# Performance work log

Hardware: AMD Instinct MI355X
Metric: run time of the kernel (lower is better)

## Reference

```python
import jax, jax.numpy as jnp
import numpy as np

ALPHA = 0.5  # init alpha
B, T, D, H = 32, 1024, 512, 512


def _cell(x, h, c, wih, whh, bih, bhh):
    # PyTorch LSTM cell: gates in i, f, g, o order
    g = x @ wih.T + bih + h @ whh.T + bhh  # (B, 4H)
    i, f, gg, o = jnp.split(g, 4, axis=-1)
    c2 = jax.nn.sigmoid(f) * c + jax.nn.sigmoid(i) * jnp.tanh(gg)
    h2 = jax.nn.sigmoid(o) * jnp.tanh(c2)
    return h2, c2


def setup_inputs() -> dict:
    key = jax.random.key(0)
    ks = jax.random.split(key, 9)
    s = 1.0 / np.sqrt(H)  # torch default init scale
    u = lambda k, shp: jax.random.uniform(k, shp, jnp.float32, -s, s)
    return {
        "u_sequence": jax.random.normal(ks[0], (B, T, D), jnp.float32),
        "w_ih_f": u(ks[1], (4 * H, D)),
        "w_hh_f": u(ks[2], (4 * H, H)),
        "b_ih_f": u(ks[3], (4 * H,)),
        "b_hh_f": u(ks[4], (4 * H,)),
        "w_ih_b": u(ks[5], (4 * H, D)),
        "w_hh_b": u(ks[6], (4 * H, H)),
        "b_ih_b": u(ks[7], (4 * H,)),
        "b_hh_b": u(ks[8], (4 * H,)),
    }


def reference(u_sequence, w_ih_f, w_hh_f, b_ih_f, b_hh_f,
              w_ih_b, w_hh_b, b_ih_b, b_hh_b):
    # Per timestep the original calls the bidirectional LSTM on a length-1
    # slice: both directions reduce to a single cell step on the same input.
    # Hidden/cell state (2, B, H) is carried across timesteps.
    pf = (w_ih_f, w_hh_f, b_ih_f, b_hh_f)
    pb = (w_ih_b, w_hh_b, b_ih_b, b_hh_b)
    Bn, Tn, Dn = u_sequence.shape
    Hn = w_hh_f.shape[1]
    z = jnp.zeros((Bn, Hn), u_sequence.dtype)

    def bi_step(x, hf, cf, hb, cb):
        hf2, cf2 = _cell(x, hf, cf, *pf)
        hb2, cb2 = _cell(x, hb, cb, *pb)
        # lstm_out[:, 0, :] == concat(h_fwd, h_bwd) for seq_len == 1
        return jnp.concatenate([hf2, hb2], axis=-1), hf2, cf2, hb2, cb2

    def step(carry, u_t):  # u_t: (B, D)
        hf, cf, hb, cb = carry
        out1, hf1, cf1, hb1, cb1 = bi_step(u_t, hf, cf, hb, cb)
        x_hat = out1[:, -1:]                 # last channel scalar, (B, 1)
        x_hat_prime = u_t + x_hat            # broadcast -> (B, D)
        out2, hf2, cf2, hb2, cb2 = bi_step(x_hat_prime, hf1, cf1, hb1, cb1)
        x_hat_next = out2[:, -1:]
        out = u_t + (1.0 - ALPHA) * x_hat_prime + ALPHA * x_hat_next
        return (hf2, cf2, hb2, cb2), out

    u_tm = jnp.swapaxes(u_sequence, 0, 1)    # (T, B, D)
    _, outs = jax.lax.scan(step, (z, z, z, z), u_tm)
    return jnp.swapaxes(outs, 0, 1)          # (B, T, D)
```

## Files before the change

### kernel.cpp

```cpp
#include <hip/hip_runtime.h>
#include <cstdint>
#include <cstddef>

#define BB 32
#define TT 1024
#define DD 512
#define HH 512
#define NBLK 64
#define NTHR 512

typedef __bf16 bf16x8 __attribute__((ext_vector_type(8)));
typedef float  f32x4  __attribute__((ext_vector_type(4)));
typedef unsigned long long u64;

#define HFRAG_OFF 0
#define XHAT_OFF  131072
#define IFLAG_OFF 393216
#define VFLAG_OFF 394240

#define AT_LOAD(p)     __hip_atomic_load((p),      __ATOMIC_RELAXED, __HIP_MEMORY_SCOPE_AGENT)
#define AT_STORE(p, v) __hip_atomic_store((p), (v), __ATOMIC_RELAXED, __HIP_MEMORY_SCOPE_AGENT)

__device__ __forceinline__ float sigm(float x) {
    return 1.f / (1.f + __expf(-x));
}
__device__ __forceinline__ float tanh_fast(float x) {
    x = fminf(15.f, fmaxf(-15.f, x));
    float e = __expf(2.f * x);
    return (e - 1.f) / (e + 1.f);
}


__device__ __forceinline__ void arrive_flag(int* iflags, int bid) {
    __builtin_amdgcn_s_waitcnt(0);
    __syncthreads();
    if (threadIdx.x == 0) AT_STORE(&iflags[bid], 1);
}
__device__ __forceinline__ void wait_flag(const int* iflags) {
    if (threadIdx.x < 64) {
        for (;;) {
            int v = AT_LOAD(&iflags[threadIdx.x]);
            if (__all(v >= 1)) break;
            __builtin_amdgcn_s_sleep(1);
        }
    }
    __syncthreads();
}

__device__ __forceinline__ void publish(int* vf, int bid, int n) {
    __builtin_amdgcn_s_waitcnt(0);
    __syncthreads();
    if (threadIdx.x == 0) AT_STORE(&vf[bid], n);
}
__device__ __forceinline__ void wait_ver(const int* vf, int n) {
    if (threadIdx.x < 64) {
        for (;;) {
            int v = AT_LOAD(&vf[threadIdx.x]);
            if (__all(v >= n)) break;
        }
    }
    __syncthreads();
}

#define UGEMM_HALF(tt, S0)                                                    \
  {                                                                           \
    const float* ub = u + (size_t)bc * (TT * DD) + (size_t)(tt) * DD + quad * 8; \
    _Pragma("unroll")                                                         \
    for (int i8 = 0; i8 < 8; ++i8) {                                          \
      const int s = (S0) + i8;                                                \
      const float4* p = (const float4*)(ub + s * 32);                         \
      float4 x0 = p[0], x1 = p[1];                                            \
      bf16x8 uf;                                                              \
      uf[0] = (__bf16)x0.x; uf[1] = (__bf16)x0.y;                             \
      uf[2] = (__bf16)x0.z; uf[3] = (__bf16)x0.w;                             \
      uf[4] = (__bf16)x1.x; uf[5] = (__bf16)x1.y;                             \
      uf[6] = (__bf16)x1.z; uf[7] = (__bf16)x1.w;                             \
      if (s & 1) un1 = __builtin_amdgcn_mfma_f32_16x16x32_bf16(wihF[s], uf, un1, 0, 0, 0); \
      else       un0 = __builtin_amdgcn_mfma_f32_16x16x32_bf16(wihF[s], uf, un0, 0, 0, 0); \
    }                                                                         \
  }

__global__ __launch_bounds__(NTHR, 1) void lstm_persistent(
    const float* __restrict__ u,
    const float* __restrict__ wih_f, const float* __restrict__ whh_f,
    const float* __restrict__ bih_f, const float* __restrict__ bhh_f,
    const float* __restrict__ wih_b, const float* __restrict__ whh_b,
    const float* __restrict__ bih_b, const float* __restrict__ bhh_b,
    unsigned short* __restrict__ hfrag, float* __restrict__ xhat,
    int* __restrict__ iflags, int* __restrict__ vflags)
{
    const int bid  = blockIdx.x;
    const int k0   = bid << 3;
    const int tid  = threadIdx.x;
    const int wid  = tid >> 6;
    const int dir  = wid >> 2;
    const int mi   = (wid >> 1) & 1;
    const int ni   = wid & 1;
    const int lane = tid & 63;
    const int quad = lane >> 4;
    const int l16  = lane & 15;

    const float* wih = dir ? wih_b : wih_f;
    const float* whh = dir ? whh_b : whh_f;
    const float* bih = dir ? bih_b : bih_f;
    const float* bhh = dir ? bhh_b : bhh_f;

    bf16x8 wihF[16], whhF[16];
    {
        const int jg = (l16 >> 2) * HH + (k0 + 4 * mi) + (l16 & 3);
        #pragma unroll
        for (int s = 0; s < 16; ++s) {
            const float* p = wih + (size_t)jg * DD + s * 32 + quad * 8;
            const float* q = whh + (size_t)jg * HH + s * 32 + quad * 8;
            bf16x8 a, b;
            #pragma unroll
            for (int i = 0; i < 8; ++i) { a[i] = (__bf16)p[i]; b[i] = (__bf16)q[i]; }
            wihF[s] = a;
            whhF[s] = b;
        }
    }

    const int kc = k0 + 4 * mi + quad;
    const int bc = ni * 16 + l16;

    float rsv[4], biasv[4];
    {
        float rs = 0.f;
        #pragma unroll
        for (int s = 0; s < 16; ++s)
            #pragma unroll
            for (int i = 0; i < 8; ++i) rs += (float)wihF[s][i];
        rs += __shfl_xor(rs, 16);
        rs += __shfl_xor(rs, 32);
        #pragma unroll
        for (int g = 0; g < 4; ++g) {
            rsv[g]   = __shfl(rs, g * 4 + quad);
            const int j = g * HH + kc;
            biasv[g] = bih[j] + bhh[j];
        }
    }

    const int sw = kc >> 5, qw = (kc >> 3) & 3, iw = kc & 7;
    const int lanew = qw * 16 + l16;
    unsigned* hfrag32 = (unsigned*)hfrag;
    const int ws32_0 = (((((dir * 2 + 0) * 2 + ni) * 16 + sw) * 64 + lanew) * 8 + iw) >> 1;
    const int ws32_1 = ws32_0 + (2 * 16 * 64 * 8 >> 1);
    const u64* h64 = (const u64*)hfrag;
    const int rbA = ((dir * 2 + 0) * 2 + ni) * 2048 + lane * 2;
    const int rbB = ((dir * 2 + 1) * 2 + ni) * 2048 + lane * 2;

    if (!(quad & 1)) AT_STORE(&hfrag32[ws32_0], 0u);
    if (bid == 0 && tid < 64) AT_STORE(&vflags[tid], 0);

    __shared__ __align__(16) float gbuf[8][16][20];

    arrive_flag(iflags, bid);
    f32x4 un0 = (f32x4){0.f, 0.f, 0.f, 0.f};
    f32x4 un1 = (f32x4){0.f, 0.f, 0.f, 0.f};
    UGEMM_HALF(0, 0);
    UGEMM_HALF(0, 8);
    wait_flag(iflags);

    f32x4 gih = un0 + un1;
    float c = 0.f;
    int n = 1;

    for (int t = 0; t < TT; ++t) {
        #pragma unroll 1
        for (int pass = 0; pass < 2; ++pass, ++n) {
            const int bufR = (t * 2 + pass) & 1;
            float xc = 0.f;
            if (pass) xc = AT_LOAD(&xhat[t * BB + bc]);

            u64 ha[16], hb[16];
            {
                const int rb = bufR ? rbB : rbA;
                #pragma unroll
                for (int s = 0; s < 16; ++s) {
                    ha[s] = AT_LOAD(&h64[rb + s * 128]);
                    hb[s] = AT_LOAD(&h64[rb + s * 128 + 1]);
                }
            }
            f32x4 acc0 = gih;
            f32x4 acc1 = (f32x4){0.f, 0.f, 0.f, 0.f};
            #pragma unroll
            for (int s = 0; s < 16; ++s) {
                union { u64 q[2]; bf16x8 v; } cvt;
                cvt.q[0] = ha[s]; cvt.q[1] = hb[s];
                if (s & 1) acc1 = __builtin_amdgcn_mfma_f32_16x16x32_bf16(whhF[s], cvt.v, acc1, 0, 0, 0);
                else       acc0 = __builtin_amdgcn_mfma_f32_16x16x32_bf16(whhF[s], cvt.v, acc0, 0, 0, 0);
            }
            f32x4 acc = acc0 + acc1;

            float4 gw; gw.x = acc[0]; gw.y = acc[1]; gw.z = acc[2]; gw.w = acc[3];
            *(float4*)&gbuf[wid][l16][quad * 4] = gw;
            __syncthreads();
            float gI = gbuf[wid][l16][ 0 + quad] + biasv[0] + xc * rsv[0];
            float gF = gbuf[wid][l16][ 4 + quad] + biasv[1] + xc * rsv[1];
            float gG = gbuf[wid][l16][ 8 + quad] + biasv[2] + xc * rsv[2];
            float gO = gbuf[wid][l16][12 + quad] + biasv[3] + xc * rsv[3];

            float ig = sigm(gI), fg = sigm(gF), gg = tanh_fast(gG), og = sigm(gO);
            c = fg * c + ig * gg;
            float h = og * tanh_fast(c);

            float hp = __shfl_xor(h, 16);
            if (dir == 1 && kc == (HH - 1))
                AT_STORE(&xhat[pass * (TT * BB) + t * BB + bc], h);
            if (!(quad & 1)) {
                unsigned lo = (unsigned)__builtin_bit_cast(unsigned short, (__bf16)h);
                unsigned hi = (unsigned)__builtin_bit_cast(unsigned short, (__bf16)hp);
                AT_STORE(&hfrag32[bufR ? ws32_0 : ws32_1], lo | (hi << 16));
            }

            publish(vflags, bid, n);
            if (t + 1 < TT) {
                if (pass == 0) {
                    un0 = (f32x4){0.f, 0.f, 0.f, 0.f};
                    un1 = (f32x4){0.f, 0.f, 0.f, 0.f};
                    UGEMM_HALF(t + 1, 0);
                } else {
                    UGEMM_HALF(t + 1, 8);
                }
            }
            wait_ver(vflags, n);
        }
        gih = un0 + un1;
    }
}

__global__ void epilogue(const float* __restrict__ u, const float* __restrict__ xhat,
                         float* __restrict__ out)
{
    const int i = blockIdx.x * blockDim.x + threadIdx.x;
    const float4 uv = ((const float4*)u)[i];
    const int bt = i >> 7;
    const int t = bt & (TT - 1);
    const int b = bt >> 10;
    const float s = 0.5f * (xhat[t * BB + b] + xhat[TT * BB + t * BB + b]);
    float4 o;
    o.x = 1.5f * uv.x + s;
    o.y = 1.5f * uv.y + s;
    o.z = 1.5f * uv.z + s;
    o.w = 1.5f * uv.w + s;
    ((float4*)out)[i] = o;
}

extern "C" void kernel_launch(void* const* d_in, const int* in_sizes, int n_in,
                              void* d_out, int out_size, void* d_ws, size_t ws_size,
                              hipStream_t stream) {
    const float* u     = (const float*)d_in[0];
    const float* wih_f = (const float*)d_in[1];
    const float* whh_f = (const float*)d_in[2];
    const float* bih_f = (const float*)d_in[3];
    const float* bhh_f = (const float*)d_in[4];
    const float* wih_b = (const float*)d_in[5];
    const float* whh_b = (const float*)d_in[6];
    const float* bih_b = (const float*)d_in[7];
    const float* bhh_b = (const float*)d_in[8];

    char* ws = (char*)d_ws;
    unsigned short* hfrag = (unsigned short*)(ws + HFRAG_OFF);
    float* xhat           = (float*)(ws + XHAT_OFF);
    int* iflags           = (int*)(ws + IFLAG_OFF);
    int* vflags           = (int*)(ws + VFLAG_OFF);

    lstm_persistent<<<NBLK, NTHR, 0, stream>>>(
        u, wih_f, whh_f, bih_f, bhh_f, wih_b, whh_b, bih_b, bhh_b,
        hfrag, xhat, iflags, vflags);

    const int n4 = BB * TT * DD / 4;
    epilogue<<<n4 / 256, 256, 0, stream>>>(u, xhat, (float*)d_out);
}
```

Before: 15.28 ms.

## Replace per-step grid barrier with NaN-sentinel data-flag polling on 4-slot ring

Removes the publish/wait_ver version-flag grid barrier each pass. Instead, hidden-state fragments and the x_hat scalar live in a 4-deep ring buffer whose slots are pre-cleared to a NaN sentinel. Readers poll the data itself until no sentinel remains, and writers clear the slot two steps ahead. This drops a barrier round trip and block-wide syncs from the recurrent critical path. In exchange it relies on the sentinel never colliding with real bf16 data and on relaxed-atomic ordering, and it polls without sleep.

```diff
diff --git a/kernel.cpp b/kernel.cpp
--- a/kernel.cpp
+++ b/kernel.cpp
@@ -13,10 +13,13 @@
 typedef float  f32x4  __attribute__((ext_vector_type(4)));
 typedef unsigned long long u64;
 
+#define CLR32  0x7FC07FC0u
+#define CLRF   0x7FC00000u
+
 #define HFRAG_OFF 0
-#define XHAT_OFF  131072
-#define IFLAG_OFF 393216
-#define VFLAG_OFF 394240
+#define XHAT_OFF  262144
+#define XRING_OFF 524288
+#define IFLAG_OFF 524800
 
 #define AT_LOAD(p)     __hip_atomic_load((p),      __ATOMIC_RELAXED, __HIP_MEMORY_SCOPE_AGENT)
 #define AT_STORE(p, v) __hip_atomic_store((p), (v), __ATOMIC_RELAXED, __HIP_MEMORY_SCOPE_AGENT)
@@ -29,7 +32,6 @@
     float e = __expf(2.f * x);
     return (e - 1.f) / (e + 1.f);
 }
-
 
 __device__ __forceinline__ void arrive_flag(int* iflags, int bid) {
     __builtin_amdgcn_s_waitcnt(0);
@@ -42,21 +44,6 @@
             int v = AT_LOAD(&iflags[threadIdx.x]);
             if (__all(v >= 1)) break;
             __builtin_amdgcn_s_sleep(1);
-        }
-    }
-    __syncthreads();
-}
-
-__device__ __forceinline__ void publish(int* vf, int bid, int n) {
-    __builtin_amdgcn_s_waitcnt(0);
-    __syncthreads();
-    if (threadIdx.x == 0) AT_STORE(&vf[bid], n);
-}
-__device__ __forceinline__ void wait_ver(const int* vf, int n) {
-    if (threadIdx.x < 64) {
-        for (;;) {
-            int v = AT_LOAD(&vf[threadIdx.x]);
-            if (__all(v >= n)) break;
         }
     }
     __syncthreads();
@@ -87,7 +74,7 @@
     const float* __restrict__ wih_b, const float* __restrict__ whh_b,
     const float* __restrict__ bih_b, const float* __restrict__ bhh_b,
     unsigned short* __restrict__ hfrag, float* __restrict__ xhat,
-    int* __restrict__ iflags, int* __restrict__ vflags)
+    unsigned* __restrict__ xring, int* __restrict__ iflags)
 {
     const int bid  = blockIdx.x;
     const int k0   = bid << 3;
@@ -143,14 +130,19 @@
     const int sw = kc >> 5, qw = (kc >> 3) & 3, iw = kc & 7;
     const int lanew = qw * 16 + l16;
     unsigned* hfrag32 = (unsigned*)hfrag;
-    const int ws32_0 = (((((dir * 2 + 0) * 2 + ni) * 16 + sw) * 64 + lanew) * 8 + iw) >> 1;
-    const int ws32_1 = ws32_0 + (2 * 16 * 64 * 8 >> 1);
+    const int ws32_rel = (((((dir) * 2 + ni) * 16 + sw) * 64 + lanew) * 8 + iw) >> 1;
     const u64* h64 = (const u64*)hfrag;
-    const int rbA = ((dir * 2 + 0) * 2 + ni) * 2048 + lane * 2;
-    const int rbB = ((dir * 2 + 1) * 2 + ni) * 2048 + lane * 2;
-
-    if (!(quad & 1)) AT_STORE(&hfrag32[ws32_0], 0u);
-    if (bid == 0 && tid < 64) AT_STORE(&vflags[tid], 0);
+
+    if (!(quad & 1)) {
+        AT_STORE(&hfrag32[0 * 16384 + ws32_rel], 0u);
+        AT_STORE(&hfrag32[1 * 16384 + ws32_rel], CLR32);
+        AT_STORE(&hfrag32[2 * 16384 + ws32_rel], CLR32);
+        AT_STORE(&hfrag32[3 * 16384 + ws32_rel], CLR32);
+    }
+    if (dir == 1 && kc == (HH - 1)) {
+        #pragma unroll
+        for (int b2 = 0; b2 < 4; ++b2) AT_STORE(&xring[b2 * BB + bc], CLRF);
+    }
 
     __shared__ __align__(16) float gbuf[8][16][20];
 
@@ -163,24 +155,39 @@
 
     f32x4 gih = un0 + un1;
     float c = 0.f;
-    int n = 1;
 
     for (int t = 0; t < TT; ++t) {
         #pragma unroll 1
-        for (int pass = 0; pass < 2; ++pass, ++n) {
-            const int bufR = (t * 2 + pass) & 1;
-            float xc = 0.f;
-            if (pass) xc = AT_LOAD(&xhat[t * BB + bc]);
+        for (int pass = 0; pass < 2; ++pass) {
+            const int n    = t * 2 + pass;
+            const int rbuf = n & 3;
+            const int wbuf = (n + 1) & 3;
+            const int cbuf = (n + 3) & 3;
 
             u64 ha[16], hb[16];
-            {
-                const int rb = bufR ? rbB : rbA;
+            unsigned rdys = 0;
+            bool xok = (pass == 0);
+            unsigned xbits = 0;
+            const int rb = ((rbuf * 2 + dir) * 2 + ni) * 2048 + lane * 2;
+            for (;;) {
                 #pragma unroll
-                for (int s = 0; s < 16; ++s) {
+                for (int s = 0; s < 16; ++s) if (!((rdys >> s) & 1)) {
                     ha[s] = AT_LOAD(&h64[rb + s * 128]);
                     hb[s] = AT_LOAD(&h64[rb + s * 128 + 1]);
                 }
-            }
+                if (!xok) xbits = AT_LOAD(&xring[rbuf * BB + bc]);
+                bool allr = true;
+                #pragma unroll
+                for (int s = 0; s < 16; ++s) if (!((rdys >> s) & 1)) {
+                    bool ok = ((unsigned)ha[s] != CLR32) && ((unsigned)(ha[s] >> 32) != CLR32)
+                           && ((unsigned)hb[s] != CLR32) && ((unsigned)(hb[s] >> 32) != CLR32);
+                    if (__all(ok)) rdys |= (1u << s); else allr = false;
+                }
+                if (!xok) { if (__all(xbits != CLRF)) xok = true; else allr = false; }
+                if (allr && xok) break;
+            }
+            const float xc = pass ? __builtin_bit_cast(float, xbits) : 0.f;
+
             f32x4 acc0 = gih;
             f32x4 acc1 = (f32x4){0.f, 0.f, 0.f, 0.f};
             #pragma unroll
@@ -205,15 +212,20 @@
             float h = og * tanh_fast(c);
 
             float hp = __shfl_xor(h, 16);
-            if (dir == 1 && kc == (HH - 1))
-                AT_STORE(&xhat[pass * (TT * BB) + t * BB + bc], h);
+            if (dir == 1 && kc == (HH - 1)) {
+                xhat[pass * (TT * BB) + t * BB + bc] = h;
+                AT_STORE(&xring[wbuf * BB + bc], __builtin_bit_cast(unsigned, h));
+            }
             if (!(quad & 1)) {
                 unsigned lo = (unsigned)__builtin_bit_cast(unsigned short, (__bf16)h);
                 unsigned hi = (unsigned)__builtin_bit_cast(unsigned short, (__bf16)hp);
-                AT_STORE(&hfrag32[bufR ? ws32_0 : ws32_1], lo | (hi << 16));
-            }
-
-            publish(vflags, bid, n);
+                AT_STORE(&hfrag32[wbuf * 16384 + ws32_rel], lo | (hi << 16));
+            }
+
+            if (!(quad & 1)) AT_STORE(&hfrag32[cbuf * 16384 + ws32_rel], CLR32);
+            if (dir == 1 && kc == (HH - 1)) AT_STORE(&xring[cbuf * BB + bc], CLRF);
+            __builtin_amdgcn_s_waitcnt(0);
+
             if (t + 1 < TT) {
                 if (pass == 0) {
                     un0 = (f32x4){0.f, 0.f, 0.f, 0.f};
@@ -223,7 +235,6 @@
                     UGEMM_HALF(t + 1, 8);
                 }
             }
-            wait_ver(vflags, n);
         }
         gih = un0 + un1;
     }
@@ -262,12 +273,12 @@
     char* ws = (char*)d_ws;
     unsigned short* hfrag = (unsigned short*)(ws + HFRAG_OFF);
     float* xhat           = (float*)(ws + XHAT_OFF);
+    unsigned* xring       = (unsigned*)(ws + XRING_OFF);
     int* iflags           = (int*)(ws + IFLAG_OFF);
-    int* vflags           = (int*)(ws + VFLAG_OFF);
 
     lstm_persistent<<<NBLK, NTHR, 0, stream>>>(
         u, wih_f, whh_f, bih_f, bhh_f, wih_b, whh_b, bih_b, bhh_b,
-        hfrag, xhat, iflags, vflags);
+        hfrag, xhat, xring, iflags);
 
     const int n4 = BB * TT * DD / 4;
     epilogue<<<n4 / 256, 256, 0, stream>>>(u, xhat, (float*)d_out);
```

Measured after the change: 20.44 ms. +33.7%, slower.

## Replace block-wide grid barriers with per-wave flags and tagged data validation

Applied to the files above, without the earlier changes.

Drops the per-pass publish/wait grid barrier, which used waitcnt plus two __syncthreads. Each wave now publishes its own version flag, and wave 0 of every block polls all 512 flags and signals the other waves through a shared-memory mailbox. The h fragments carry a parity bit stolen from the bf16 mantissa LSB and the xhat scalar carries a 3-bit timestep tag in a ring, so readers spin until the data is valid rather than relying purely on ordering. The __syncthreads before the LDS gate exchange is replaced by an lgkmcnt wait. This trades barrier latency for extra polling traffic, slight precision loss from the tag bits, and subtle memory-ordering risks.

```diff
diff --git a/kernel.cpp b/kernel.cpp
--- a/kernel.cpp
+++ b/kernel.cpp
@@ -15,11 +15,13 @@
 
 #define HFRAG_OFF 0
 #define XHAT_OFF  131072
-#define IFLAG_OFF 393216
-#define VFLAG_OFF 394240
+#define XRING_OFF 393216
+#define IFLAG_OFF 393472
+#define VFLAG_OFF 393728
 
 #define AT_LOAD(p)     __hip_atomic_load((p),      __ATOMIC_RELAXED, __HIP_MEMORY_SCOPE_AGENT)
 #define AT_STORE(p, v) __hip_atomic_store((p), (v), __ATOMIC_RELAXED, __HIP_MEMORY_SCOPE_AGENT)
+
 
 __device__ __forceinline__ float sigm(float x) {
     return 1.f / (1.f + __expf(-x));
@@ -29,7 +31,6 @@
     float e = __expf(2.f * x);
     return (e - 1.f) / (e + 1.f);
 }
-
 
 __device__ __forceinline__ void arrive_flag(int* iflags, int bid) {
     __builtin_amdgcn_s_waitcnt(0);
@@ -47,29 +48,14 @@
     __syncthreads();
 }
 
-__device__ __forceinline__ void publish(int* vf, int bid, int n) {
-    __builtin_amdgcn_s_waitcnt(0);
-    __syncthreads();
-    if (threadIdx.x == 0) AT_STORE(&vf[bid], n);
-}
-__device__ __forceinline__ void wait_ver(const int* vf, int n) {
-    if (threadIdx.x < 64) {
-        for (;;) {
-            int v = AT_LOAD(&vf[threadIdx.x]);
-            if (__all(v >= n)) break;
-        }
-    }
-    __syncthreads();
-}
-
 #define UGEMM_HALF(tt, S0)                                                    \
   {                                                                           \
     const float* ub = u + (size_t)bc * (TT * DD) + (size_t)(tt) * DD + quad * 8; \
     _Pragma("unroll")                                                         \
     for (int i8 = 0; i8 < 8; ++i8) {                                          \
       const int s = (S0) + i8;                                                \
-      const float4* p = (const float4*)(ub + s * 32);                         \
-      float4 x0 = p[0], x1 = p[1];                                            \
+      const float4* pp4 = (const float4*)(ub + s * 32);                       \
+      float4 x0 = pp4[0], x1 = pp4[1];                                        \
       bf16x8 uf;                                                              \
       uf[0] = (__bf16)x0.x; uf[1] = (__bf16)x0.y;                             \
       uf[2] = (__bf16)x0.z; uf[3] = (__bf16)x0.w;                             \
@@ -87,7 +73,8 @@
     const float* __restrict__ wih_b, const float* __restrict__ whh_b,
     const float* __restrict__ bih_b, const float* __restrict__ bhh_b,
     unsigned short* __restrict__ hfrag, float* __restrict__ xhat,
-    int* __restrict__ iflags, int* __restrict__ vflags)
+    unsigned* __restrict__ xring, int* __restrict__ iflags,
+    int* __restrict__ vflags)
 {
     const int bid  = blockIdx.x;
     const int k0   = bid << 3;
@@ -149,10 +136,19 @@
     const int rbA = ((dir * 2 + 0) * 2 + ni) * 2048 + lane * 2;
     const int rbB = ((dir * 2 + 1) * 2 + ni) * 2048 + lane * 2;
 
-    if (!(quad & 1)) AT_STORE(&hfrag32[ws32_0], 0u);
-    if (bid == 0 && tid < 64) AT_STORE(&vflags[tid], 0);
+    if (!(quad & 1)) {
+        AT_STORE(&hfrag32[ws32_0], 0u);
+        AT_STORE(&hfrag32[ws32_1], 0x00000001u);
+    }
+    if (dir == 1 && kc == (HH - 1)) {
+        AT_STORE(&xring[0 * BB + bc], 0x7FC00001u);
+        AT_STORE(&xring[1 * BB + bc], 0x7FC00000u);
+    }
+    if (bid == 0) AT_STORE(&vflags[tid], 0);
 
     __shared__ __align__(16) float gbuf[8][16][20];
+    volatile __shared__ int mbox;
+    if (tid == 0) mbox = 0;
 
     arrive_flag(iflags, bid);
     f32x4 un0 = (f32x4){0.f, 0.f, 0.f, 0.f};
@@ -163,38 +159,74 @@
 
     f32x4 gih = un0 + un1;
     float c = 0.f;
-    int n = 1;
+    const u64 vmask = 0x0000000100000001ULL;
 
     for (int t = 0; t < TT; ++t) {
         #pragma unroll 1
-        for (int pass = 0; pass < 2; ++pass, ++n) {
-            const int bufR = (t * 2 + pass) & 1;
+        for (int pass = 0; pass < 2; ++pass) {
+            const int np = t * 2 + pass;
+
+            if (np) {
+                if (wid == 0) {
+                    const u64* vf64 = (const u64*)vflags;
+                    for (;;) {
+                        u64 a0 = AT_LOAD(&vf64[lane]);
+                        u64 a1 = AT_LOAD(&vf64[lane + 64]);
+                        u64 a2 = AT_LOAD(&vf64[lane + 128]);
+                        u64 a3 = AT_LOAD(&vf64[lane + 192]);
+                        bool ok = ((int)a0 >= np) & ((int)(a0 >> 32) >= np)
+                                & ((int)a1 >= np) & ((int)(a1 >> 32) >= np)
+                                & ((int)a2 >= np) & ((int)(a2 >> 32) >= np)
+                                & ((int)a3 >= np) & ((int)(a3 >> 32) >= np);
+                        if (__all(ok)) break;
+                    }
+                    if (lane == 0) mbox = np;
+                } else {
+                    while (mbox < np) { }
+                }
+            }
+
             float xc = 0.f;
-            if (pass) xc = AT_LOAD(&xhat[t * BB + bc]);
-
-            u64 ha[16], hb[16];
+            if (pass) {
+                unsigned xb;
+                for (;;) {
+                    xb = AT_LOAD(&xring[(t & 1) * BB + bc]);
+                    if (__all((xb & 7u) == (unsigned)(t & 7))) break;
+                }
+                xc = __builtin_bit_cast(float, xb);
+            }
+
+            f32x4 acc0, acc1;
             {
-                const int rb = bufR ? rbB : rbA;
-                #pragma unroll
-                for (int s = 0; s < 16; ++s) {
-                    ha[s] = AT_LOAD(&h64[rb + s * 128]);
-                    hb[s] = AT_LOAD(&h64[rb + s * 128 + 1]);
-                }
-            }
-            f32x4 acc0 = gih;
-            f32x4 acc1 = (f32x4){0.f, 0.f, 0.f, 0.f};
-            #pragma unroll
-            for (int s = 0; s < 16; ++s) {
-                union { u64 q[2]; bf16x8 v; } cvt;
-                cvt.q[0] = ha[s]; cvt.q[1] = hb[s];
-                if (s & 1) acc1 = __builtin_amdgcn_mfma_f32_16x16x32_bf16(whhF[s], cvt.v, acc1, 0, 0, 0);
-                else       acc0 = __builtin_amdgcn_mfma_f32_16x16x32_bf16(whhF[s], cvt.v, acc0, 0, 0, 0);
+                const int rb    = (np & 1) ? rbB : rbA;
+                const u64 gmask = ((np >> 1) & 1) ? vmask : 0ULL;
+                for (;;) {
+                    u64 ha[16], hb[16];
+                    #pragma unroll
+                    for (int s = 0; s < 16; ++s) {
+                        ha[s] = AT_LOAD(&h64[rb + s * 128]);
+                        hb[s] = AT_LOAD(&h64[rb + s * 128 + 1]);
+                    }
+                    u64 bad0 = 0, bad1 = 0;
+                    acc0 = gih;
+                    acc1 = (f32x4){0.f, 0.f, 0.f, 0.f};
+                    #pragma unroll
+                    for (int s = 0; s < 16; ++s) {
+                        bad0 |= (ha[s] ^ gmask) & vmask;
+                        bad1 |= (hb[s] ^ gmask) & vmask;
+                        union { u64 q[2]; bf16x8 v; } cvt;
+                        cvt.q[0] = ha[s]; cvt.q[1] = hb[s];
+                        if (s & 1) acc1 = __builtin_amdgcn_mfma_f32_16x16x32_bf16(whhF[s], cvt.v, acc1, 0, 0, 0);
+                        else       acc0 = __builtin_amdgcn_mfma_f32_16x16x32_bf16(whhF[s], cvt.v, acc0, 0, 0, 0);
+                    }
+                    if (__all((bad0 | bad1) == 0ULL)) break;
+                }
             }
             f32x4 acc = acc0 + acc1;
 
-            float4 gw; gw.x = acc[0]; gw.y = acc[1]; gw.z = acc[2]; gw.w = acc[3];
-            *(float4*)&gbuf[wid][l16][quad * 4] = gw;
-            __syncthreads();
+            float4 gv; gv.x = acc[0]; gv.y = acc[1]; gv.z = acc[2]; gv.w = acc[3];
+            *(float4*)&gbuf[wid][l16][quad * 4] = gv;
+            asm volatile("s_waitcnt lgkmcnt(0)" ::: "memory");
             float gI = gbuf[wid][l16][ 0 + quad] + biasv[0] + xc * rsv[0];
             float gF = gbuf[wid][l16][ 4 + quad] + biasv[1] + xc * rsv[1];
             float gG = gbuf[wid][l16][ 8 + quad] + biasv[2] + xc * rsv[2];
@@ -204,16 +236,26 @@
             c = fg * c + ig * gg;
             float h = og * tanh_fast(c);
 
+            const unsigned gw = (unsigned)(((np + 1) >> 1) & 1);
             float hp = __shfl_xor(h, 16);
-            if (dir == 1 && kc == (HH - 1))
-                AT_STORE(&xhat[pass * (TT * BB) + t * BB + bc], h);
+            if (dir == 1 && kc == (HH - 1)) {
+                xhat[pass * (TT * BB) + t * BB + bc] = h;
+                if (pass == 0) {
+                    const unsigned xb = (__builtin_bit_cast(unsigned, h) & ~7u)
+                                      | (unsigned)(t & 7);
+                    AT_STORE(&xring[(t & 1) * BB + bc], xb);
+                }
+            }
             if (!(quad & 1)) {
                 unsigned lo = (unsigned)__builtin_bit_cast(unsigned short, (__bf16)h);
                 unsigned hi = (unsigned)__builtin_bit_cast(unsigned short, (__bf16)hp);
-                AT_STORE(&hfrag32[bufR ? ws32_0 : ws32_1], lo | (hi << 16));
-            }
-
-            publish(vflags, bid, n);
+                lo = (lo & ~1u) | gw;
+                AT_STORE(&hfrag32[((np + 1) & 1) ? ws32_1 : ws32_0], lo | (hi << 16));
+            }
+            __builtin_amdgcn_sched_barrier(0);
+            if (lane == 0) AT_STORE(&vflags[(bid << 3) + wid], np + 1);
+            __builtin_amdgcn_sched_barrier(0);
+
             if (t + 1 < TT) {
                 if (pass == 0) {
                     un0 = (f32x4){0.f, 0.f, 0.f, 0.f};
@@ -223,7 +265,6 @@
                     UGEMM_HALF(t + 1, 8);
                 }
             }
-            wait_ver(vflags, n);
         }
         gih = un0 + un1;
     }
@@ -262,12 +303,13 @@
     char* ws = (char*)d_ws;
     unsigned short* hfrag = (unsigned short*)(ws + HFRAG_OFF);
     float* xhat           = (float*)(ws + XHAT_OFF);
+    unsigned* xring       = (unsigned*)(ws + XRING_OFF);
     int* iflags           = (int*)(ws + IFLAG_OFF);
     int* vflags           = (int*)(ws + VFLAG_OFF);
 
     lstm_persistent<<<NBLK, NTHR, 0, stream>>>(
         u, wih_f, whh_f, bih_f, bhh_f, wih_b, whh_b, bih_b, bhh_b,
-        hfrag, xhat, iflags, vflags);
+        hfrag, xhat, xring, iflags, vflags);
 
     const int n4 = BB * TT * DD / 4;
     epilogue<<<n4 / 256, 256, 0, stream>>>(u, xhat, (float*)d_out);
```

Result: slower. 16.43 ms (+7.5%).
